# Performance work log

Hardware: AMD Instinct MI355X
Metric: run time of the kernel (lower is better)

Reference implementation:

```python
import jax, jax.numpy as jnp
import numpy as np

NFREQ = 5


def setup_inputs() -> dict:
    key = jax.random.key(0)
    k1, k2 = jax.random.split(key)
    B, H, T, F = 16, 16, 1024, 64
    x = jax.random.normal(k1, (B, H, T, F), dtype=jnp.float32)
    # Conv3D kernel: (1, k0, k1, in_ch=F, out_ch=F) as in keras DHWIO layout
    W = jax.random.normal(k2, (1, 3, 3, F, F), dtype=jnp.float32) * 0.05
    b = jnp.zeros((F,), dtype=jnp.float32)
    return {"x": x, "W": W, "b": b}


def _conv3d_relu(x5, W, b):
    # x5: [B, H, P, Q, F]; W: [1, k0, k1, F, F]; 'same' padding, stride 1
    y = jax.lax.conv_general_dilated(
        x5, W, window_strides=(1, 1, 1), padding='SAME',
        dimension_numbers=('NDHWC', 'DHWIO', 'NDHWC'))
    return jax.nn.relu(y + b)


def reference(x, W, b):
    B, H, T, F = x.shape
    freq_list = np.arange(1, T // 2, T // 2 // NFREQ)  # static python ints
    # amplitude: |rfft over T|, mean over F -> [B, H, T//2+1]
    amp = jnp.mean(jnp.abs(jnp.fft.rfft(x, axis=2)), axis=-1)
    period_weight = amp[:, :, freq_list]              # [B, H, nfreq]
    pw = jax.nn.softmax(period_weight, axis=-1)       # [B, H, nfreq]

    res = []
    for p in (freq_list + 1):
        p = int(p)
        q = int(np.ceil(T / p))                       # segments per period
        pad = q * p - T
        xt = jnp.pad(x, ((0, 0), (0, 0), (0, pad), (0, 0)))
        x5 = xt.reshape(B, H, p, q, F)                # [B,H,p,q,F]
        y = _conv3d_relu(x5, W, b)                    # [B,H,p,q,F]
        y = y.reshape(B, H, p * q, F)[:, :, :T, :]    # crop back to T
        res.append(y)
    res = jnp.stack(res, axis=-1)                     # [B,H,T,F,nfreq]
    out = jnp.sum(res * pw[:, :, None, None, :], axis=-1) + x
    return out
```

## Files before the change

kernel.cpp:

```cpp
#include <hip/hip_runtime.h>

typedef __attribute__((ext_vector_type(8))) short bhalf8;
typedef __attribute__((ext_vector_type(4))) float floatx4;

#define NF 6

__device__ __forceinline__ unsigned short f2bf(float f) {
  unsigned u = __float_as_uint(f);
  u += 0x7FFFu + ((u >> 16) & 1u);
  return (unsigned short)(u >> 16);
}

__global__ __launch_bounds__(512) void pw_kernel(const float* __restrict__ x,
                                                 float* __restrict__ pwbuf,
                                                 const float* __restrict__ W,
                                                 unsigned short* __restrict__ wt_img) {
  const int tid = threadIdx.x;
  if (blockIdx.x >= 256) {
    if (tid < 256) {
      int task = (blockIdx.x - 256) * 256 + tid;
      int didj = task >> 9;
      int fo = (task >> 3) & 63;
      int c = task & 7;
      int cs = c ^ (fo & 7);
      bhalf8 pk;
#pragma unroll
      for (int j = 0; j < 8; ++j) {
        int fi = cs * 8 + j;
        pk[j] = (short)f2bf(W[(size_t)(didj * 64 + fi) * 64 + fo]);
      }
      *(bhalf8*)((char*)wt_img + (size_t)didj * 8192 + fo * 128 + c * 16) = pk;
    }
    return;
  }
  const int bh = blockIdx.x;
  const int w = tid >> 6;
  const int f = tid & 63;
  const int t0w = w * 128;
  const float* xb = x + (size_t)bh * 65536 + f;

  const float STEP = -6.283185307179586f / 1024.0f;
  float re[NF], im[NF], c[NF], s[NF], ck[NF], sk[NF];
#pragma unroll
  for (int k = 0; k < NF; ++k) {
    int freq = 1 + 102 * k;
    int ph0 = (freq * t0w) & 1023;
    __sincosf((float)ph0 * STEP, &s[k], &c[k]);
    __sincosf((float)freq * STEP, &sk[k], &ck[k]);
    re[k] = 0.f;
    im[k] = 0.f;
  }
#pragma unroll 4
  for (int t = 0; t < 128; ++t) {
    float v = xb[(size_t)(t0w + t) * 64];
#pragma unroll
    for (int k = 0; k < NF; ++k) {
      re[k] = fmaf(v, c[k], re[k]);
      im[k] = fmaf(v, s[k], im[k]);
      float cn = fmaf(c[k], ck[k], -s[k] * sk[k]);
      float sn = fmaf(c[k], sk[k], s[k] * ck[k]);
      c[k] = cn;
      s[k] = sn;
    }
  }
  __shared__ float part[8][NF][64][2];
#pragma unroll
  for (int k = 0; k < NF; ++k) {
    part[w][k][f][0] = re[k];
    part[w][k][f][1] = im[k];
  }
  __syncthreads();
  if (tid < 64) {
    float sm[NF];
#pragma unroll
    for (int k = 0; k < NF; ++k) {
      float rr = 0.f, ii = 0.f;
#pragma unroll
      for (int ww = 0; ww < 8; ++ww) {
        rr += part[ww][k][tid][0];
        ii += part[ww][k][tid][1];
      }
      float amp = sqrtf(rr * rr + ii * ii);
#pragma unroll
      for (int off = 32; off > 0; off >>= 1) amp += __shfl_xor(amp, off);
      sm[k] = amp * (1.0f / 64.0f);
    }
    if (tid == 0) {
      float m = sm[0];
#pragma unroll
      for (int i = 1; i < NF; ++i) m = fmaxf(m, sm[i]);
      float e[NF], ssum = 0.f;
#pragma unroll
      for (int i = 0; i < NF; ++i) {
        e[i] = __expf(sm[i] - m);
        ssum += e[i];
      }
      float inv = 1.0f / ssum;
#pragma unroll
      for (int i = 0; i < NF; ++i) pwbuf[bh * NF + i] = e[i] * inv;
    }
  }
}

__global__ __launch_bounds__(512, 2) void conv_kernel(
    const float* __restrict__ x, const unsigned short* __restrict__ wt_img,
    const float* __restrict__ bias, const float* __restrict__ pwbuf,
    float* __restrict__ out) {
  __shared__ __align__(16) unsigned short win[2][152 * 64];
  __shared__ __align__(16) unsigned short wl[9 * 64 * 64];
  __shared__ __align__(16) unsigned short zrow[64];

  const int tid = threadIdx.x;
  const int bh = blockIdx.y;
  const int t0 = blockIdx.x * 128;
  const float* xbh = x + (size_t)bh * (1024 * 64);

  {
    const int fi0 = (tid & 7) * 8;
#pragma unroll
    for (int w = 0; w < 2; ++w) {
      int tbase = w * 512 + t0 - 12;
#pragma unroll
      for (int rr = 0; rr < 3; ++rr) {
        int trel = (tid >> 3) + rr * 64;
        if (trel < 152) {
          int tp = tbase + trel;
          float va[8];
          if ((unsigned)tp < 1024u) {
            const float4* src = (const float4*)(xbh + (size_t)tp * 64 + fi0);
            float4 u0 = src[0], u1 = src[1];
            va[0] = u0.x; va[1] = u0.y; va[2] = u0.z; va[3] = u0.w;
            va[4] = u1.x; va[5] = u1.y; va[6] = u1.z; va[7] = u1.w;
          } else {
#pragma unroll
            for (int j = 0; j < 8; ++j) va[j] = 0.f;
          }
          bhalf8 pk;
#pragma unroll
          for (int j = 0; j < 8; ++j) pk[j] = (short)f2bf(va[j]);
          *(bhalf8*)((char*)win[w] + (trel << 7) +
                     ((fi0 * 2) ^ ((trel & 7) << 4))) = pk;
        }
      }
    }
#pragma unroll
    for (int d = 0; d < 9; ++d) {
      const char* src = (const char*)wt_img + (size_t)d * 8192;
      char* dst = (char*)wl + (size_t)d * 8192;
      *(bhalf8*)(dst + tid * 16) = *(const bhalf8*)(src + tid * 16);
    }
    if (tid < 8) *(bhalf8*)((char*)zrow + tid * 16) = (bhalf8)0;
  }
  __syncthreads();

  const int l15 = tid & 15;
  const int l4x16 = ((tid >> 4) & 3) * 16;
  const int wid = tid >> 6;
  const int g = wid >> 2;
  const int wr = wid & 3;
  const int rtb = g * 512 + t0 + wr * 32;
  const int dOther = g ? 0 : 2;
  const char* ownw = (const char*)win[g];
  const char* othw = (const char*)win[1 - g];
  const char* zb = (const char*)zrow;

  const int rt0 = rtb + l15, rt1 = rt0 + 16;
  int eLo0 = 0, eHi0 = 0, eLo1 = 0, eHi1 = 0;
  {
    int j0, j1;
    j0 = rt0 & 511; j1 = rt1 & 511;
    eLo0 |= (j0 == 0) << 0;   eHi0 |= (j0 == 511) << 0;
    eLo1 |= (j1 == 0) << 0;   eHi1 |= (j1 == 511) << 0;
    j0 = rt0 % 10;  j1 = rt1 % 10;
    eLo0 |= (j0 == 0) << 1;   eHi0 |= (j0 == 9) << 1;
    eLo1 |= (j1 == 0) << 1;   eHi1 |= (j1 == 9) << 1;
    j0 = rt0 % 5;   j1 = rt1 % 5;
    eLo0 |= (j0 == 0) << 2;   eHi0 |= (j0 == 4) << 2;
    eLo1 |= (j1 == 0) << 2;   eHi1 |= (j1 == 4) << 2;
    j0 = rt0 & 3;   j1 = rt1 & 3;
    eLo0 |= (j0 == 0) << 3;   eHi0 |= (j0 == 3) << 3;
    eLo1 |= (j1 == 0) << 3;   eHi1 |= (j1 == 3) << 3;
    j0 = rt0 % 3;   j1 = rt1 % 3;
    eLo0 |= (j0 == 0) << 4;   eHi0 |= (j0 == 2) << 4;
    eLo1 |= (j1 == 0) << 4;   eHi1 |= (j1 == 2) << 4;
    j0 = rt0 & 1;   j1 = rt1 & 1;
    eLo0 |= (j0 == 0) << 5;   eHi0 |= (j0 == 1) << 5;
    eLo1 |= (j1 == 0) << 5;   eHi1 |= (j1 == 1) << 5;
  }

  float pwv[NF];
#pragma unroll
  for (int kp = 0; kp < NF; ++kp) pwv[kp] = pwbuf[bh * NF + kp];
  float bv[4];
#pragma unroll
  for (int nt = 0; nt < 4; ++nt) bv[nt] = bias[nt * 16 + l15];

  floatx4 fin[2][4];
#pragma unroll
  for (int mt = 0; mt < 2; ++mt)
#pragma unroll
    for (int nt = 0; nt < 4; ++nt) fin[mt][nt] = (floatx4)0.0f;

  const int base = wr * 32 + l15;

#define DO_TAP(C, KP, BUFBASE, R0)                                            \
  {                                                                           \
    int r0_ = (R0), r1_ = r0_ + 16;                                           \
    const char* pa0 = (((bad0 >> (KP)) & 1) == 0)                             \
                          ? (const char*)(BUFBASE) + (r0_ << 7) : zb;         \
    const char* pa1 = (((bad1 >> (KP)) & 1) == 0)                             \
                          ? (const char*)(BUFBASE) + (r1_ << 7) : zb;         \
    int sw0 = (r0_ & 7) << 4, sw1 = (r1_ & 7) << 4;                           \
    _Pragma("unroll") for (int kk = 0; kk < 2; ++kk) {                        \
      int kb = kk * 64 + l4x16;                                               \
      bhalf8 a0 = *(const bhalf8*)(pa0 + (kb ^ sw0));                         \
      bhalf8 a1 = *(const bhalf8*)(pa1 + (kb ^ sw1));                         \
      _Pragma("unroll") for (int nt = 0; nt < 4; ++nt) {                      \
        acc[C][0][nt] = __builtin_amdgcn_mfma_f32_16x16x32_bf16(              \
            a0, bfr[kk][nt], acc[C][0][nt], 0, 0, 0);                         \
        acc[C][1][nt] = __builtin_amdgcn_mfma_f32_16x16x32_bf16(              \
            a1, bfr[kk][nt], acc[C][1][nt], 0, 0, 0);                         \
      }                                                                       \
    }                                                                         \
  }

#define LOAD_BFR                                                              \
  bhalf8 bfr[2][4];                                                           \
  {                                                                           \
    const char* wt = (const char*)wl + (size_t)(di * 3 + dj) * 8192;          \
    _Pragma("unroll") for (int kk = 0; kk < 2; ++kk)                          \
        _Pragma("unroll") for (int nt = 0; nt < 4; ++nt) {                    \
      int fo = nt * 16 + l15;                                                 \
      bfr[kk][nt] = *(const bhalf8*)(wt + (fo << 7) +                         \
                                     ((kk * 64 + l4x16) ^ ((fo & 7) << 4)));  \
    }                                                                         \
  }

#define FOLD(C, KP)                                                           \
  _Pragma("unroll") for (int mt = 0; mt < 2; ++mt)                            \
      _Pragma("unroll") for (int nt = 0; nt < 4; ++nt)                        \
          _Pragma("unroll") for (int r = 0; r < 4; ++r)                       \
              fin[mt][nt][r] = fmaf(                                          \
                  pwv[KP], fmaxf(acc[C][mt][nt][r] + bv[nt], 0.f),            \
                  fin[mt][nt][r]);

  {
    floatx4 acc[3][2][4];
#pragma unroll
    for (int c = 0; c < 3; ++c)
#pragma unroll
      for (int mt = 0; mt < 2; ++mt)
#pragma unroll
        for (int nt = 0; nt < 4; ++nt) acc[c][mt][nt] = (floatx4)0.0f;
#pragma unroll 1
    for (int di = 0; di < 3; ++di) {
#pragma unroll
      for (int dj = 0; dj < 3; ++dj) {
        LOAD_BFR
        int bad0 = (dj == 0) ? eLo0 : (dj == 2) ? eHi0 : 0;
        int bad1 = (dj == 0) ? eLo1 : (dj == 2) ? eHi1 : 0;
        if (di == 1) {
          DO_TAP(0, 0, ownw, base + 11 + dj)
        } else if (di == dOther) {
          DO_TAP(0, 0, othw, base + 11 + dj)
        }
        const int so = di - 1;
        DO_TAP(1, 1, ownw, base + 12 + so * 10 + dj - 1)
        DO_TAP(2, 2, ownw, base + 12 + so * 5 + dj - 1)
      }
    }
    FOLD(0, 0) FOLD(1, 1) FOLD(2, 2)
  }

  {
    floatx4 acc[3][2][4];
#pragma unroll
    for (int c = 0; c < 3; ++c)
#pragma unroll
      for (int mt = 0; mt < 2; ++mt)
#pragma unroll
        for (int nt = 0; nt < 4; ++nt) acc[c][mt][nt] = (floatx4)0.0f;
#pragma unroll 1
    for (int di = 0; di < 3; ++di) {
#pragma unroll
      for (int dj = 0; dj < 3; ++dj) {
        LOAD_BFR
        int bad0 = (dj == 0) ? eLo0 : (dj == 2) ? eHi0 : 0;
        int bad1 = (dj == 0) ? eLo1 : (dj == 2) ? eHi1 : 0;
        const int so = di - 1;
        DO_TAP(0, 3, ownw, base + 12 + so * 4 + dj - 1)
        DO_TAP(1, 4, ownw, base + 12 + so * 3 + dj - 1)
        DO_TAP(2, 5, ownw, base + 12 + so * 2 + dj - 1)
      }
    }
    FOLD(0, 3) FOLD(1, 4) FOLD(2, 5)
  }
#undef DO_TAP
#undef LOAD_BFR
#undef FOLD

#pragma unroll
  for (int mt = 0; mt < 2; ++mt) {
#pragma unroll
    for (int nt = 0; nt < 4; ++nt) {
      int row = rtb + mt * 16 + ((tid >> 4) & 3) * 4;
      int col = nt * 16 + l15;
      size_t basep = ((size_t)bh * 1024 + row) * 64 + col;
#pragma unroll
      for (int r = 0; r < 4; ++r) {
        out[basep + (size_t)r * 64] =
            fin[mt][nt][r] + x[basep + (size_t)r * 64];
      }
    }
  }
}

extern "C" void kernel_launch(void* const* d_in, const int* in_sizes, int n_in,
                              void* d_out, int out_size, void* d_ws,
                              size_t ws_size, hipStream_t stream) {
  const float* x = (const float*)d_in[0];
  const float* W = (const float*)d_in[1];
  const float* b = (const float*)d_in[2];
  float* out = (float*)d_out;
  float* pwbuf = (float*)d_ws;
  unsigned short* wt_img = (unsigned short*)((char*)d_ws + 8192);

  pw_kernel<<<dim3(256 + 18), dim3(512), 0, stream>>>(x, pwbuf, W, wt_img);
  conv_kernel<<<dim3(4, 256), dim3(512), 0, stream>>>(x, wt_img, b, pwbuf, out);
}
```

Measured before the change: 122.4 us.

## Double conv block size to 1024 threads with one M-tile per wave

The conv kernel now launches 1024 threads per block, and each wave handles 16 rows instead of 32. This halves the accumulator registers per thread and doubles the number of waves sharing the same LDS window and weight tile. In exchange, each wave reloads the B fragments from LDS for only half as many MFMAs, which raises LDS traffic per FLOP. The block's LDS footprint stays the same, so residency moves from two 512-thread blocks per CU to one 1024-thread block.

```diff
diff --git a/kernel.cpp b/kernel.cpp
--- a/kernel.cpp
+++ b/kernel.cpp
@@ -102,7 +102,7 @@
   }
 }
 
-__global__ __launch_bounds__(512, 2) void conv_kernel(
+__global__ __launch_bounds__(1024, 1) void conv_kernel(
     const float* __restrict__ x, const unsigned short* __restrict__ wt_img,
     const float* __restrict__ bias, const float* __restrict__ pwbuf,
     float* __restrict__ out) {
@@ -121,8 +121,8 @@
     for (int w = 0; w < 2; ++w) {
       int tbase = w * 512 + t0 - 12;
 #pragma unroll
-      for (int rr = 0; rr < 3; ++rr) {
-        int trel = (tid >> 3) + rr * 64;
+      for (int rr = 0; rr < 2; ++rr) {
+        int trel = (tid >> 3) + rr * 128;
         if (trel < 152) {
           int tp = tbase + trel;
           float va[8];
@@ -143,12 +143,8 @@
         }
       }
     }
-#pragma unroll
-    for (int d = 0; d < 9; ++d) {
-      const char* src = (const char*)wt_img + (size_t)d * 8192;
-      char* dst = (char*)wl + (size_t)d * 8192;
-      *(bhalf8*)(dst + tid * 16) = *(const bhalf8*)(src + tid * 16);
-    }
+    for (int c = tid; c < 4608; c += 1024)
+      ((bhalf8*)wl)[c] = ((const bhalf8*)wt_img)[c];
     if (tid < 8) *(bhalf8*)((char*)zrow + tid * 16) = (bhalf8)0;
   }
   __syncthreads();
@@ -156,36 +152,24 @@
   const int l15 = tid & 15;
   const int l4x16 = ((tid >> 4) & 3) * 16;
   const int wid = tid >> 6;
-  const int g = wid >> 2;
-  const int wr = wid & 3;
-  const int rtb = g * 512 + t0 + wr * 32;
+  const int g = wid >> 3;
+  const int wr = wid & 7;
+  const int rtb = g * 512 + t0 + wr * 16;
   const int dOther = g ? 0 : 2;
   const char* ownw = (const char*)win[g];
   const char* othw = (const char*)win[1 - g];
   const char* zb = (const char*)zrow;
 
-  const int rt0 = rtb + l15, rt1 = rt0 + 16;
-  int eLo0 = 0, eHi0 = 0, eLo1 = 0, eHi1 = 0;
-  {
-    int j0, j1;
-    j0 = rt0 & 511; j1 = rt1 & 511;
-    eLo0 |= (j0 == 0) << 0;   eHi0 |= (j0 == 511) << 0;
-    eLo1 |= (j1 == 0) << 0;   eHi1 |= (j1 == 511) << 0;
-    j0 = rt0 % 10;  j1 = rt1 % 10;
-    eLo0 |= (j0 == 0) << 1;   eHi0 |= (j0 == 9) << 1;
-    eLo1 |= (j1 == 0) << 1;   eHi1 |= (j1 == 9) << 1;
-    j0 = rt0 % 5;   j1 = rt1 % 5;
-    eLo0 |= (j0 == 0) << 2;   eHi0 |= (j0 == 4) << 2;
-    eLo1 |= (j1 == 0) << 2;   eHi1 |= (j1 == 4) << 2;
-    j0 = rt0 & 3;   j1 = rt1 & 3;
-    eLo0 |= (j0 == 0) << 3;   eHi0 |= (j0 == 3) << 3;
-    eLo1 |= (j1 == 0) << 3;   eHi1 |= (j1 == 3) << 3;
-    j0 = rt0 % 3;   j1 = rt1 % 3;
-    eLo0 |= (j0 == 0) << 4;   eHi0 |= (j0 == 2) << 4;
-    eLo1 |= (j1 == 0) << 4;   eHi1 |= (j1 == 2) << 4;
-    j0 = rt0 & 1;   j1 = rt1 & 1;
-    eLo0 |= (j0 == 0) << 5;   eHi0 |= (j0 == 1) << 5;
-    eLo1 |= (j1 == 0) << 5;   eHi1 |= (j1 == 1) << 5;
+  const int rt0 = rtb + l15;
+  int eLo0 = 0, eHi0 = 0;
+  {
+    int j0;
+    j0 = rt0 & 511;  eLo0 |= (j0 == 0) << 0;  eHi0 |= (j0 == 511) << 0;
+    j0 = rt0 % 10;   eLo0 |= (j0 == 0) << 1;  eHi0 |= (j0 == 9) << 1;
+    j0 = rt0 % 5;    eLo0 |= (j0 == 0) << 2;  eHi0 |= (j0 == 4) << 2;
+    j0 = rt0 & 3;    eLo0 |= (j0 == 0) << 3;  eHi0 |= (j0 == 3) << 3;
+    j0 = rt0 % 3;    eLo0 |= (j0 == 0) << 4;  eHi0 |= (j0 == 2) << 4;
+    j0 = rt0 & 1;    eLo0 |= (j0 == 0) << 5;  eHi0 |= (j0 == 1) << 5;
   }
 
   float pwv[NF];
@@ -195,39 +179,33 @@
 #pragma unroll
   for (int nt = 0; nt < 4; ++nt) bv[nt] = bias[nt * 16 + l15];
 
-  floatx4 fin[2][4];
-#pragma unroll
-  for (int mt = 0; mt < 2; ++mt)
-#pragma unroll
-    for (int nt = 0; nt < 4; ++nt) fin[mt][nt] = (floatx4)0.0f;
-
-  const int base = wr * 32 + l15;
+  floatx4 fin[4];
+#pragma unroll
+  for (int nt = 0; nt < 4; ++nt) fin[nt] = (floatx4)0.0f;
+
+  const int base = wr * 16 + l15;
+
+#define MFMA16(A, B, C) __builtin_amdgcn_mfma_f32_16x16x32_bf16((A), (B), (C), 0, 0, 0)
 
 #define DO_TAP(C, KP, BUFBASE, R0)                                            \
   {                                                                           \
-    int r0_ = (R0), r1_ = r0_ + 16;                                           \
+    int r0_ = (R0);                                                           \
     const char* pa0 = (((bad0 >> (KP)) & 1) == 0)                             \
                           ? (const char*)(BUFBASE) + (r0_ << 7) : zb;         \
-    const char* pa1 = (((bad1 >> (KP)) & 1) == 0)                             \
-                          ? (const char*)(BUFBASE) + (r1_ << 7) : zb;         \
-    int sw0 = (r0_ & 7) << 4, sw1 = (r1_ & 7) << 4;                           \
+    int sw_ = (r0_ & 7) << 4;                                                 \
     _Pragma("unroll") for (int kk = 0; kk < 2; ++kk) {                        \
       int kb = kk * 64 + l4x16;                                               \
-      bhalf8 a0 = *(const bhalf8*)(pa0 + (kb ^ sw0));                         \
-      bhalf8 a1 = *(const bhalf8*)(pa1 + (kb ^ sw1));                         \
+      bhalf8 a0 = *(const bhalf8*)(pa0 + (kb ^ sw_));                         \
       _Pragma("unroll") for (int nt = 0; nt < 4; ++nt) {                      \
-        acc[C][0][nt] = __builtin_amdgcn_mfma_f32_16x16x32_bf16(              \
-            a0, bfr[kk][nt], acc[C][0][nt], 0, 0, 0);                         \
-        acc[C][1][nt] = __builtin_amdgcn_mfma_f32_16x16x32_bf16(              \
-            a1, bfr[kk][nt], acc[C][1][nt], 0, 0, 0);                         \
+        acc[C][nt] = MFMA16(a0, bfr[kk][nt], acc[C][nt]);                     \
       }                                                                       \
     }                                                                         \
   }
 
-#define LOAD_BFR                                                              \
+#define LOAD_BFR(DI, DJ)                                                      \
   bhalf8 bfr[2][4];                                                           \
   {                                                                           \
-    const char* wt = (const char*)wl + (size_t)(di * 3 + dj) * 8192;          \
+    const char* wt = (const char*)wl + (size_t)((DI) * 3 + (DJ)) * 8192;      \
     _Pragma("unroll") for (int kk = 0; kk < 2; ++kk)                          \
         _Pragma("unroll") for (int nt = 0; nt < 4; ++nt) {                    \
       int fo = nt * 16 + l15;                                                 \
@@ -237,28 +215,23 @@
   }
 
 #define FOLD(C, KP)                                                           \
-  _Pragma("unroll") for (int mt = 0; mt < 2; ++mt)                            \
-      _Pragma("unroll") for (int nt = 0; nt < 4; ++nt)                        \
-          _Pragma("unroll") for (int r = 0; r < 4; ++r)                       \
-              fin[mt][nt][r] = fmaf(                                          \
-                  pwv[KP], fmaxf(acc[C][mt][nt][r] + bv[nt], 0.f),            \
-                  fin[mt][nt][r]);
-
-  {
-    floatx4 acc[3][2][4];
+  _Pragma("unroll") for (int nt = 0; nt < 4; ++nt)                            \
+      _Pragma("unroll") for (int r = 0; r < 4; ++r)                           \
+          fin[nt][r] = fmaf(pwv[KP], fmaxf(acc[C][nt][r] + bv[nt], 0.f),      \
+                            fin[nt][r]);
+
+  {
+    floatx4 acc[3][4];
 #pragma unroll
     for (int c = 0; c < 3; ++c)
 #pragma unroll
-      for (int mt = 0; mt < 2; ++mt)
-#pragma unroll
-        for (int nt = 0; nt < 4; ++nt) acc[c][mt][nt] = (floatx4)0.0f;
+      for (int nt = 0; nt < 4; ++nt) acc[c][nt] = (floatx4)0.0f;
 #pragma unroll 1
     for (int di = 0; di < 3; ++di) {
 #pragma unroll
       for (int dj = 0; dj < 3; ++dj) {
-        LOAD_BFR
+        LOAD_BFR(di, dj)
         int bad0 = (dj == 0) ? eLo0 : (dj == 2) ? eHi0 : 0;
-        int bad1 = (dj == 0) ? eLo1 : (dj == 2) ? eHi1 : 0;
         if (di == 1) {
           DO_TAP(0, 0, ownw, base + 11 + dj)
         } else if (di == dOther) {
@@ -273,20 +246,17 @@
   }
 
   {
-    floatx4 acc[3][2][4];
+    floatx4 acc[3][4];
 #pragma unroll
     for (int c = 0; c < 3; ++c)
 #pragma unroll
-      for (int mt = 0; mt < 2; ++mt)
-#pragma unroll
-        for (int nt = 0; nt < 4; ++nt) acc[c][mt][nt] = (floatx4)0.0f;
+      for (int nt = 0; nt < 4; ++nt) acc[c][nt] = (floatx4)0.0f;
 #pragma unroll 1
     for (int di = 0; di < 3; ++di) {
 #pragma unroll
       for (int dj = 0; dj < 3; ++dj) {
-        LOAD_BFR
+        LOAD_BFR(di, dj)
         int bad0 = (dj == 0) ? eLo0 : (dj == 2) ? eHi0 : 0;
-        int bad1 = (dj == 0) ? eLo1 : (dj == 2) ? eHi1 : 0;
         const int so = di - 1;
         DO_TAP(0, 3, ownw, base + 12 + so * 4 + dj - 1)
         DO_TAP(1, 4, ownw, base + 12 + so * 3 + dj - 1)
@@ -298,19 +268,16 @@
 #undef DO_TAP
 #undef LOAD_BFR
 #undef FOLD
-
-#pragma unroll
-  for (int mt = 0; mt < 2; ++mt) {
-#pragma unroll
-    for (int nt = 0; nt < 4; ++nt) {
-      int row = rtb + mt * 16 + ((tid >> 4) & 3) * 4;
-      int col = nt * 16 + l15;
-      size_t basep = ((size_t)bh * 1024 + row) * 64 + col;
-#pragma unroll
-      for (int r = 0; r < 4; ++r) {
-        out[basep + (size_t)r * 64] =
-            fin[mt][nt][r] + x[basep + (size_t)r * 64];
-      }
+#undef MFMA16
+
+#pragma unroll
+  for (int nt = 0; nt < 4; ++nt) {
+    int row = rtb + ((tid >> 4) & 3) * 4;
+    int col = nt * 16 + l15;
+    size_t basep = ((size_t)bh * 1024 + row) * 64 + col;
+#pragma unroll
+    for (int r = 0; r < 4; ++r) {
+      out[basep + (size_t)r * 64] = fin[nt][r] + x[basep + (size_t)r * 64];
     }
   }
 }
@@ -326,5 +293,5 @@
   unsigned short* wt_img = (unsigned short*)((char*)d_ws + 8192);
 
   pw_kernel<<<dim3(256 + 18), dim3(512), 0, stream>>>(x, pwbuf, W, wt_img);
-  conv_kernel<<<dim3(4, 256), dim3(512), 0, stream>>>(x, wt_img, b, pwbuf, out);
-}
+  conv_kernel<<<dim3(4, 256), dim3(1024), 0, stream>>>(x, wt_img, b, pwbuf, out);
+}
```

Result: slower. 154.4 us (+26.2%).
